# Optimization experiments

Measured on AMD Instinct MI355X. Metric: run time of the kernel, lower is better.

The kernel has to match this reference:

```python
import jax, jax.numpy as jnp
from jax import lax
import numpy as np

NPOINT = 2048
NSAMPLE = 16
LEAKY = 0.1


def _leaky(x):
    return jnp.where(x >= 0, x, LEAKY * x)


def _fps(pts, npoint):
    # pts: [B, N, 3] -> idx [B, npoint] (furthest point sampling, start at index 0)
    B, N, _ = pts.shape

    def step(carry, _):
        dist, far = carry  # dist [B,N], far [B]
        c = jnp.take_along_axis(pts, far[:, None, None], axis=1)  # [B,1,3]
        d = jnp.sum((pts - c) ** 2, -1)  # [B,N]
        dist = jnp.minimum(dist, d)
        nxt = jnp.argmax(dist, -1).astype(jnp.int32)
        return (dist, nxt), far

    init = (jnp.full((B, N), 1e10, pts.dtype), jnp.zeros((B,), jnp.int32))
    _, idx = lax.scan(step, init, None, length=npoint)
    return jnp.transpose(idx)  # [B, npoint]


def setup_inputs() -> dict:
    key = jax.random.key(0)
    ks = jax.random.split(key, 6)
    B, N, D, O = 8, 8192, 64, 128
    xyz = jax.random.normal(ks[0], (B, 3, N), jnp.float32)
    points = jax.random.normal(ks[1], (B, D, N), jnp.float32)
    W_kernel = jax.random.normal(ks[2], (O, D + 3), jnp.float32) * 0.05
    W_linear = jax.random.normal(ks[3], (O + NSAMPLE, O + NSAMPLE), jnp.float32) * 0.05
    W_point = jax.random.normal(ks[4], (NSAMPLE, NSAMPLE), jnp.float32) * 0.05
    W_channel = jax.random.normal(ks[5], (O, O), jnp.float32) * 0.05
    return {"xyz": xyz, "points": points, "W_kernel": W_kernel,
            "W_linear": W_linear, "W_point": W_point, "W_channel": W_channel}


def reference(xyz, points, W_kernel, W_linear, W_point, W_channel):
    K, S = NSAMPLE, NPOINT
    xyz_t = jnp.transpose(xyz, (0, 2, 1))      # [B,N,3]
    pts_t = jnp.transpose(points, (0, 2, 1))   # [B,N,D]

    fps_idx = _fps(xyz_t, S)                   # [B,S]
    new_xyz = jax.vmap(lambda p, i: p[i])(xyz_t, fps_idx)  # [B,S,3]

    # KNN: squared distances new_xyz -> xyz
    d = (jnp.sum(new_xyz ** 2, -1)[:, :, None]
         + jnp.sum(xyz_t ** 2, -1)[:, None, :]
         - 2.0 * jnp.einsum('bsc,bnc->bsn', new_xyz, xyz_t))  # [B,S,N]
    _, knn = lax.top_k(-d, K)                  # [B,S,K]

    gxyz = jax.vmap(lambda p, i: p[i])(xyz_t, knn)          # [B,S,K,3]
    gxyz_n = gxyz - new_xyz[:, :, None, :]
    gpts = jax.vmap(lambda p, i: p[i])(pts_t, knn)          # [B,S,K,D]
    new_points = jnp.concatenate([gxyz_n, gpts], -1)        # [B,S,K,3+D]

    # 1x1 conv2d kernel + LeakyReLU
    feat = _leaky(jnp.einsum('oc,bskc->bosk', W_kernel, new_points))  # [B,O,S,K]

    ch_avg = jnp.mean(feat, -1)                # [B,O,S]
    pt_avg = jnp.mean(feat, 1)                 # [B,S,K]
    agg = jnp.concatenate([ch_avg, jnp.transpose(pt_avg, (0, 2, 1))], 1)  # [B,O+K,S]
    agg = _leaky(jnp.einsum('oc,bcs->bos', W_linear, agg))

    wp = jax.nn.sigmoid(jnp.einsum('oc,bcs->bos', W_point, agg[:, -K:]))   # [B,K,S]
    wc = jax.nn.sigmoid(jnp.einsum('oc,bcs->bos', W_channel, agg[:, :-K]))  # [B,O,S]

    gated = feat * wc[:, :, :, None] * jnp.transpose(wp, (0, 2, 1))[:, None, :, :]
    out = jnp.mean(gated, -1)                  # [B,O,S]
    return jnp.transpose(new_xyz, (0, 2, 1)), out, fps_idx
```

## Files before the change

kernel.cpp:

```cpp
#include <hip/hip_runtime.h>
#include <stdint.h>

#define NB 8
#define NPT 8192
#define ND 64
#define NO 128
#define NS 2048
#define NK 16
#define NCONS 248
#define NITER 67

typedef float f32x2 __attribute__((ext_vector_type(2)));

constexpr int WS_PTS_T  = 0;
constexpr int WS_XYZW   = WS_PTS_T + NB*NPT*ND;
constexpr int WS_GFAR   = WS_XYZW + NB*NPT*4;
constexpr int WS_SYNC   = WS_GFAR + NB*NS;

constexpr int OUT_NEWXYZ = 0;
constexpr int OUT_FEAT   = NB*3*NS;
constexpr int OUT_FPS    = OUT_FEAT + NB*NO*NS;

__device__ __forceinline__ float sq3(float x, float y, float z) {
#pragma clang fp contract(off)
  return (x*x + y*y) + z*z;
}

__device__ __forceinline__ f32x2 fps_d2(f32x2 px, f32x2 py, f32x2 pz, f32x2 cx, f32x2 cy, f32x2 cz) {
#pragma clang fp contract(off)
  f32x2 dx = px - cx, dy = py - cy, dz = pz - cz;
  return (dx*dx + dy*dy) + dz*dz;
}

__device__ __forceinline__ float knn_d(float qn, float pn,
                                       float qx,float qy,float qz,
                                       float px,float py,float pz) {
#pragma clang fp contract(off)
  float dot = (qx*px + qy*py) + qz*pz;
  return (qn + pn) - 2.0f*dot;
}

__device__ __forceinline__ float wave_max_dpp(float x) {
  int v;
  v = __builtin_amdgcn_update_dpp(__float_as_int(x), __float_as_int(x), 0x111, 0xF, 0xF, false);
  x = fmaxf(x, __int_as_float(v));
  v = __builtin_amdgcn_update_dpp(__float_as_int(x), __float_as_int(x), 0x112, 0xF, 0xF, false);
  x = fmaxf(x, __int_as_float(v));
  v = __builtin_amdgcn_update_dpp(__float_as_int(x), __float_as_int(x), 0x114, 0xF, 0xF, false);
  x = fmaxf(x, __int_as_float(v));
  v = __builtin_amdgcn_update_dpp(__float_as_int(x), __float_as_int(x), 0x118, 0xF, 0xF, false);
  x = fmaxf(x, __int_as_float(v));
  v = __builtin_amdgcn_update_dpp(__float_as_int(x), __float_as_int(x), 0x142, 0xA, 0xF, false);
  x = fmaxf(x, __int_as_float(v));
  v = __builtin_amdgcn_update_dpp(__float_as_int(x), __float_as_int(x), 0x143, 0xC, 0xF, false);
  x = fmaxf(x, __int_as_float(v));
  return x;
}

__global__ void k_init(float* __restrict__ ws) {
  if (threadIdx.x < 9*32) ((int*)(ws + WS_SYNC))[threadIdx.x] = 0;
}

struct MegaShared {
  union {
    struct {
      float lx[NPT], ly[NPT], lz[NPT];
      unsigned long long wred[2][8];
    } f;
    struct { float tile[64][65]; } tr;
    struct {
      float W[128*69];
      union {
        float dist[NPT];
        struct { float np[16*69]; float ft[16*132]; float chred[256]; float ptred[16*17]; } p2;
      } u;
      unsigned long long kred[8];
      int selIdx[16];
      float agg[144];
      float a2[144];
      float gates[144];
    } c;
  } u;
};

__global__ __launch_bounds__(512) void k_mega(const float* __restrict__ xyz,
                                              const float* __restrict__ points,
                                              const float* __restrict__ Wkern,
                                              const float* __restrict__ Wlin,
                                              const float* __restrict__ Wpt,
                                              const float* __restrict__ Wch,
                                              float* __restrict__ ws,
                                              float* __restrict__ dout) {
  __shared__ MegaShared sh;
  const int bid = blockIdx.x, t = threadIdx.x;
  int* syncp = (int*)(ws + WS_SYNC);
  int* gfar  = (int*)(ws + WS_GFAR);

  if (bid < NB) {
    const float* xb = xyz + (size_t)bid*3*NPT;
    f32x2 px2[8], py2[8], pz2[8], dist2[8];
    const int base = t << 4;
#pragma unroll
    for (int jj = 0; jj < 4; jj++) {
      float4 vx = *reinterpret_cast<const float4*>(xb + base + jj*4);
      float4 vy = *reinterpret_cast<const float4*>(xb + NPT + base + jj*4);
      float4 vz = *reinterpret_cast<const float4*>(xb + 2*NPT + base + jj*4);
      px2[jj*2+0] = f32x2{vx.x, vx.y}; px2[jj*2+1] = f32x2{vx.z, vx.w};
      py2[jj*2+0] = f32x2{vy.x, vy.y}; py2[jj*2+1] = f32x2{vy.z, vy.w};
      pz2[jj*2+0] = f32x2{vz.x, vz.y}; pz2[jj*2+1] = f32x2{vz.z, vz.w};
      dist2[jj*2+0] = f32x2{1e10f, 1e10f}; dist2[jj*2+1] = f32x2{1e10f, 1e10f};
      sh.u.f.lx[base+jj*4+0]=vx.x; sh.u.f.lx[base+jj*4+1]=vx.y; sh.u.f.lx[base+jj*4+2]=vx.z; sh.u.f.lx[base+jj*4+3]=vx.w;
      sh.u.f.ly[base+jj*4+0]=vy.x; sh.u.f.ly[base+jj*4+1]=vy.y; sh.u.f.ly[base+jj*4+2]=vy.z; sh.u.f.ly[base+jj*4+3]=vy.w;
      sh.u.f.lz[base+jj*4+0]=vz.x; sh.u.f.lz[base+jj*4+1]=vz.y; sh.u.f.lz[base+jj*4+2]=vz.z; sh.u.f.lz[base+jj*4+3]=vz.w;
    }
    __syncthreads();

    int far = 0;
    int* gfb = gfar + (size_t)bid*NS;

    for (int s = 0; s < NS; s++) {
      float cx = sh.u.f.lx[far], cy = sh.u.f.ly[far], cz = sh.u.f.lz[far];
      if (t == 0) {
        gfb[s] = far;
        if ((s & 31) == 31)
          __hip_atomic_store(&syncp[bid*32], s+1, __ATOMIC_RELEASE, __HIP_MEMORY_SCOPE_AGENT);
      }
      const f32x2 c2x = {cx, cx}, c2y = {cy, cy}, c2z = {cz, cz};
      float bv = -1.0f; int bi = base;
#pragma unroll
      for (int j = 0; j < 8; j++) {
        f32x2 dd = fps_d2(px2[j], py2[j], pz2[j], c2x, c2y, c2z);
        float n0 = fminf(dist2[j].x, dd.x);
        float n1 = fminf(dist2[j].y, dd.y);
        dist2[j].x = n0; dist2[j].y = n1;
        if (n0 > bv) { bv = n0; bi = base + 2*j; }
        if (n1 > bv) { bv = n1; bi = base + 2*j + 1; }
      }
      float wm = wave_max_dpp(bv);
      float wmax = __int_as_float(__builtin_amdgcn_readlane(__float_as_int(wm), 63));
      unsigned long long eq = __ballot(bv == wmax);
      int winner = __ffsll((unsigned long long)eq) - 1;
      int wbi = __builtin_amdgcn_readlane(bi, winner);
      const int par = s & 1;
      if ((t & 63) == 0)
        sh.u.f.wred[par][t >> 6] = ((unsigned long long)__float_as_uint(wmax) << 32) | (unsigned)wbi;
      __syncthreads();
      unsigned long long best = sh.u.f.wred[par][0];
#pragma unroll
      for (int w = 1; w < 8; w++) {
        unsigned long long k2 = sh.u.f.wred[par][w];
        if ((unsigned)(k2 >> 32) > (unsigned)(best >> 32)) best = k2;
      }
      far = (int)(best & 0xFFFFFFFFull);
    }
    if (t == 0)
      __hip_atomic_store(&syncp[bid*32], NS, __ATOMIC_RELEASE, __HIP_MEMORY_SCOPE_AGENT);
    return;
  }

  const int cbid = bid - NB;

  for (int tile = cbid; tile < 1024; tile += NCONS) {
    const int b  = tile >> 7;
    const int n0 = (tile & 127) << 6;
    const float* pb = points + (size_t)b*ND*NPT;
    {
      int dR = t >> 3, cg = t & 7;
      const float* src = pb + (size_t)dR*NPT + n0 + cg*8;
      float4 v0 = *reinterpret_cast<const float4*>(src);
      float4 v1 = *reinterpret_cast<const float4*>(src + 4);
      sh.u.tr.tile[dR][cg*8+0]=v0.x; sh.u.tr.tile[dR][cg*8+1]=v0.y;
      sh.u.tr.tile[dR][cg*8+2]=v0.z; sh.u.tr.tile[dR][cg*8+3]=v0.w;
      sh.u.tr.tile[dR][cg*8+4]=v1.x; sh.u.tr.tile[dR][cg*8+5]=v1.y;
      sh.u.tr.tile[dR][cg*8+6]=v1.z; sh.u.tr.tile[dR][cg*8+7]=v1.w;
    }
    __syncthreads();
    {
      int nl = t >> 3, dg = t & 7;
      float4 w0, w1;
      w0.x = sh.u.tr.tile[dg*8+0][nl]; w0.y = sh.u.tr.tile[dg*8+1][nl];
      w0.z = sh.u.tr.tile[dg*8+2][nl]; w0.w = sh.u.tr.tile[dg*8+3][nl];
      w1.x = sh.u.tr.tile[dg*8+4][nl]; w1.y = sh.u.tr.tile[dg*8+5][nl];
      w1.z = sh.u.tr.tile[dg*8+6][nl]; w1.w = sh.u.tr.tile[dg*8+7][nl];
      float* dst = ws + WS_PTS_T + ((size_t)b*NPT + n0 + nl)*ND + dg*8;
      *reinterpret_cast<float4*>(dst)     = w0;
      *reinterpret_cast<float4*>(dst + 4) = w1;
    }
    __syncthreads();
  }
  for (int chunk = cbid; chunk < 128; chunk += NCONS) {
    int g = chunk*512 + t;
    int b = g >> 13, n = g & 8191;
    const float* xb = xyz + (size_t)b*3*NPT;
    float x = xb[n], y = xb[NPT+n], z = xb[2*NPT+n];
    float4 v; v.x=x; v.y=y; v.z=z; v.w=sq3(x,y,z);
    *reinterpret_cast<float4*>(ws + WS_XYZW + (size_t)g*4) = v;
  }
  __syncthreads();
  if (t == 0) {
    __hip_atomic_fetch_add(&syncp[8*32], 1, __ATOMIC_ACQ_REL, __HIP_MEMORY_SCOPE_AGENT);
    while (__hip_atomic_load(&syncp[8*32], __ATOMIC_RELAXED, __HIP_MEMORY_SCOPE_AGENT) < NCONS)
      __builtin_amdgcn_s_sleep(8);
    (void)__hip_atomic_load(&syncp[8*32], __ATOMIC_ACQUIRE, __HIP_MEMORY_SCOPE_AGENT);
  }
  __syncthreads();

  for (int g = t; g < 128*67; g += 512) {
    int o = g / 67, c = g - o*67;
    sh.u.c.W[o*69+c] = Wkern[g];
  }
  __syncthreads();

  for (int j = 0; j < NITER; j++) {
    const int i = cbid + j*NCONS;
    const bool active = (i < NB*NS);
    const int ii = active ? i : (NB*NS - 1);
    const int b = ii & 7, s = ii >> 3;

    if (t == 0) {
      while (__hip_atomic_load(&syncp[b*32], __ATOMIC_RELAXED, __HIP_MEMORY_SCOPE_AGENT) < s+1)
        __builtin_amdgcn_s_sleep(8);
      (void)__hip_atomic_load(&syncp[b*32], __ATOMIC_ACQUIRE, __HIP_MEMORY_SCOPE_AGENT);
    }
    __syncthreads();

    const float* xyzw = ws + WS_XYZW + (size_t)b*NPT*4;
    const int far = gfar[(size_t)b*NS + s];
    const float4 q = *reinterpret_cast<const float4*>(xyzw + (size_t)far*4);

    if (active) {
      if (t == 3) dout[OUT_FPS + (size_t)b*NS + s] = (float)far;
      else if (t < 3) dout[OUT_NEWXYZ + (size_t)b*3*NS + (size_t)t*NS + s] = (t==0) ? q.x : (t==1) ? q.y : q.z;
    }

#pragma unroll
    for (int i2 = 0; i2 < 16; i2++) {
      int n = t + (i2 << 9);
      float4 p = *reinterpret_cast<const float4*>(xyzw + (size_t)n*4);
      sh.u.c.u.dist[n] = knn_d(q.w, p.w, q.x, q.y, q.z, p.x, p.y, p.z);
    }
    __syncthreads();

    for (int r = 0; r < NK; r++) {
      float bv = __int_as_float(0x7F800000); int bi = NPT;
#pragma unroll
      for (int i2 = 0; i2 < 16; i2++) {
        int n = t + (i2 << 9);
        float v = sh.u.c.u.dist[n];
        if (v < bv) { bv = v; bi = n; }
      }
      unsigned uu = __float_as_uint(bv);
      uu ^= ((unsigned)((int)uu >> 31)) | 0x80000000u;
      unsigned long long key = ((unsigned long long)uu << 32) | (unsigned)bi;
#pragma unroll
      for (int m = 1; m < 64; m <<= 1) {
        unsigned long long o = __shfl_xor(key, m, 64);
        key = (o < key) ? o : key;
      }
      if ((t & 63) == 0) sh.u.c.kred[t >> 6] = key;
      __syncthreads();
      if (t == 0) {
        unsigned long long kmin = sh.u.c.kred[0];
#pragma unroll
        for (int w = 1; w < 8; w++) { unsigned long long o = sh.u.c.kred[w]; if (o < kmin) kmin = o; }
        int win = (int)(kmin & 0xFFFFFFFFull);
        sh.u.c.selIdx[r] = win;
        sh.u.c.u.dist[win] = __int_as_float(0x7F800000);
      }
      __syncthreads();
    }

    if (t < 256) {
      int k = t >> 4, cg = t & 15;
      int idx = sh.u.c.selIdx[k];
      float4 f = *reinterpret_cast<const float4*>(ws + WS_PTS_T + ((size_t)b*NPT + idx)*ND + cg*4);
      float* nprow = sh.u.c.u.p2.np + k*69;
      nprow[3+cg*4+0]=f.x; nprow[3+cg*4+1]=f.y; nprow[3+cg*4+2]=f.z; nprow[3+cg*4+3]=f.w;
      if (cg == 0) {
        float4 g4 = *reinterpret_cast<const float4*>(xyzw + (size_t)idx*4);
        nprow[0]=g4.x-q.x; nprow[1]=g4.y-q.y; nprow[2]=g4.z-q.z;
      }
    }
    __syncthreads();

    if (t < 256) {
      const int o = t & 127, khalf = t >> 7, k0 = khalf*8;
      float acc[8] = {0,0,0,0,0,0,0,0};
      const float* Wrow = sh.u.c.W + o*69;
      for (int c = 0; c < 67; c++) {
        float w = Wrow[c];
#pragma unroll
        for (int kk = 0; kk < 8; kk++)
          acc[kk] = fmaf(w, sh.u.c.u.p2.np[(k0+kk)*69 + c], acc[kk]);
      }
      float chp = 0.f;
#pragma unroll
      for (int kk = 0; kk < 8; kk++) {
        float a = acc[kk]; a = (a >= 0.f) ? a : 0.1f*a;
        sh.u.c.u.p2.ft[(k0+kk)*132 + o] = a; chp += a;
      }
      sh.u.c.u.p2.chred[khalf*128 + o] = chp;
    }
    __syncthreads();

    if (t < 128) sh.u.c.agg[t] = (sh.u.c.u.p2.chred[t] + sh.u.c.u.p2.chred[128+t]) * 0.0625f;
    if (t < 256) {
      int k = t & 15, og = t >> 4;
      float pp = 0.f;
#pragma unroll
      for (int jj = 0; jj < 8; jj++) pp += sh.u.c.u.p2.ft[k*132 + og*8 + jj];
      sh.u.c.u.p2.ptred[k*17 + og] = pp;
    }
    __syncthreads();
    if (t < 16) {
      float pv = 0.f;
#pragma unroll
      for (int og = 0; og < 16; og++) pv += sh.u.c.u.p2.ptred[t*17 + og];
      sh.u.c.agg[128 + t] = pv * 0.0078125f;
    }
    __syncthreads();

    if (t < 144) {
      float a = 0.f;
      const float* wr = Wlin + t*144;
      for (int c = 0; c < 144; c++) a = fmaf(wr[c], sh.u.c.agg[c], a);
      sh.u.c.a2[t] = (a >= 0.f) ? a : 0.1f*a;
    }
    __syncthreads();

    if (t < 128) {
      float a = 0.f;
      const float* wr = Wch + t*128;
      for (int c = 0; c < 128; c++) a = fmaf(wr[c], sh.u.c.a2[c], a);
      sh.u.c.gates[t] = 1.f / (1.f + expf(-a));
    } else if (t < 144) {
      int o = t - 128;
      float a = 0.f;
      const float* wr = Wpt + o*16;
      for (int c = 0; c < 16; c++) a = fmaf(wr[c], sh.u.c.a2[128+c], a);
      sh.u.c.gates[t] = 1.f / (1.f + expf(-a));
    }
    __syncthreads();

    if (t < 128 && active) {
      float sum = 0.f;
#pragma unroll
      for (int k = 0; k < 16; k++)
        sum = fmaf(sh.u.c.u.p2.ft[k*132 + t], sh.u.c.gates[128 + k], sum);
      dout[OUT_FEAT + ((size_t)b*NO + t)*NS + s] = sum * sh.u.c.gates[t] * 0.0625f;
    }
    __syncthreads();
  }
}

extern "C" void kernel_launch(void* const* d_in, const int* in_sizes, int n_in,
                              void* d_out, int out_size, void* d_ws, size_t ws_size,
                              hipStream_t stream) {
  (void)in_sizes; (void)n_in; (void)out_size; (void)ws_size;
  const float* xyz    = (const float*)d_in[0];
  const float* points = (const float*)d_in[1];
  const float* Wk     = (const float*)d_in[2];
  const float* Wl     = (const float*)d_in[3];
  const float* Wp     = (const float*)d_in[4];
  const float* Wc     = (const float*)d_in[5];
  float* ws  = (float*)d_ws;
  float* out = (float*)d_out;

  hipLaunchKernelGGL(k_init, dim3(1), dim3(512), 0, stream, ws);

  void* args[] = { (void*)&xyz, (void*)&points, (void*)&Wk, (void*)&Wl,
                   (void*)&Wp, (void*)&Wc, (void*)&ws, (void*)&out };
  hipLaunchCooperativeKernel(reinterpret_cast<void*>(k_mega),
                             dim3(NB + NCONS), dim3(512), args, 0, stream);
}
```

Baseline: 2.048 ms.

## Streamline FPS loop and signal consumers per sample via sentinel-initialized index array

The FPS producer now stores each selected index directly with a relaxed atomic into a gfar array pre-filled with -1. Consumers poll that slot instead of a batched counter, so they can start on each sample as soon as it exists rather than waiting for groups of 32. The FPS inner loop also changes: coordinates are kept as float4 records in LDS, a plain max reduction is followed by a separate argmax pass, and the cross-wave reduction uses DPP plus a ballot instead of a serial loop. Risks include memory-ordering subtleties from relaxed publishing and changed tie-breaking semantics.

```diff
diff --git a/kernel.cpp b/kernel.cpp
--- a/kernel.cpp
+++ b/kernel.cpp
@@ -57,14 +57,27 @@
   return x;
 }
 
+__device__ __forceinline__ float dpp8_max(float x) {
+  int v;
+  v = __builtin_amdgcn_update_dpp(__float_as_int(x), __float_as_int(x), 0x111, 0xF, 0xF, false);
+  x = fmaxf(x, __int_as_float(v));
+  v = __builtin_amdgcn_update_dpp(__float_as_int(x), __float_as_int(x), 0x112, 0xF, 0xF, false);
+  x = fmaxf(x, __int_as_float(v));
+  v = __builtin_amdgcn_update_dpp(__float_as_int(x), __float_as_int(x), 0x114, 0xF, 0xF, false);
+  x = fmaxf(x, __int_as_float(v));
+  return x;
+}
+
 __global__ void k_init(float* __restrict__ ws) {
-  if (threadIdx.x < 9*32) ((int*)(ws + WS_SYNC))[threadIdx.x] = 0;
+  int idx = blockIdx.x*512 + threadIdx.x;
+  if (idx < NB*NS) ((int*)(ws + WS_GFAR))[idx] = -1;
+  if (idx < 32)    ((int*)(ws + WS_SYNC))[idx] = 0;
 }
 
 struct MegaShared {
   union {
     struct {
-      float lx[NPT], ly[NPT], lz[NPT];
+      float lxyz[NPT][4];
       unsigned long long wred[2][8];
     } f;
     struct { float tile[64][65]; } tr;
@@ -79,6 +92,7 @@
       float agg[144];
       float a2[144];
       float gates[144];
+      int farSlot;
     } c;
   } u;
 };
@@ -109,9 +123,14 @@
       py2[jj*2+0] = f32x2{vy.x, vy.y}; py2[jj*2+1] = f32x2{vy.z, vy.w};
       pz2[jj*2+0] = f32x2{vz.x, vz.y}; pz2[jj*2+1] = f32x2{vz.z, vz.w};
       dist2[jj*2+0] = f32x2{1e10f, 1e10f}; dist2[jj*2+1] = f32x2{1e10f, 1e10f};
-      sh.u.f.lx[base+jj*4+0]=vx.x; sh.u.f.lx[base+jj*4+1]=vx.y; sh.u.f.lx[base+jj*4+2]=vx.z; sh.u.f.lx[base+jj*4+3]=vx.w;
-      sh.u.f.ly[base+jj*4+0]=vy.x; sh.u.f.ly[base+jj*4+1]=vy.y; sh.u.f.ly[base+jj*4+2]=vy.z; sh.u.f.ly[base+jj*4+3]=vy.w;
-      sh.u.f.lz[base+jj*4+0]=vz.x; sh.u.f.lz[base+jj*4+1]=vz.y; sh.u.f.lz[base+jj*4+2]=vz.z; sh.u.f.lz[base+jj*4+3]=vz.w;
+      float xs[4] = {vx.x, vx.y, vx.z, vx.w};
+      float ys[4] = {vy.x, vy.y, vy.z, vy.w};
+      float zs[4] = {vz.x, vz.y, vz.z, vz.w};
+#pragma unroll
+      for (int i = 0; i < 4; i++) {
+        float4 rec; rec.x = xs[i]; rec.y = ys[i]; rec.z = zs[i]; rec.w = 0.f;
+        *reinterpret_cast<float4*>(&sh.u.f.lxyz[base + jj*4 + i][0]) = rec;
+      }
     }
     __syncthreads();
 
@@ -119,22 +138,29 @@
     int* gfb = gfar + (size_t)bid*NS;
 
     for (int s = 0; s < NS; s++) {
-      float cx = sh.u.f.lx[far], cy = sh.u.f.ly[far], cz = sh.u.f.lz[far];
-      if (t == 0) {
-        gfb[s] = far;
-        if ((s & 31) == 31)
-          __hip_atomic_store(&syncp[bid*32], s+1, __ATOMIC_RELEASE, __HIP_MEMORY_SCOPE_AGENT);
-      }
-      const f32x2 c2x = {cx, cx}, c2y = {cy, cy}, c2z = {cz, cz};
-      float bv = -1.0f; int bi = base;
+      if (t == 0)
+        __hip_atomic_store(&gfb[s], far, __ATOMIC_RELAXED, __HIP_MEMORY_SCOPE_AGENT);
+
+      const float4 c4 = *reinterpret_cast<const float4*>(&sh.u.f.lxyz[far][0]);
+      const f32x2 c2x = {c4.x, c4.x}, c2y = {c4.y, c4.y}, c2z = {c4.z, c4.z};
+
+      f32x2 vmax2 = {-1.0f, -1.0f};
 #pragma unroll
       for (int j = 0; j < 8; j++) {
         f32x2 dd = fps_d2(px2[j], py2[j], pz2[j], c2x, c2y, c2z);
-        float n0 = fminf(dist2[j].x, dd.x);
-        float n1 = fminf(dist2[j].y, dd.y);
-        dist2[j].x = n0; dist2[j].y = n1;
-        if (n0 > bv) { bv = n0; bi = base + 2*j; }
-        if (n1 > bv) { bv = n1; bi = base + 2*j + 1; }
+        f32x2 nd;
+        nd.x = fminf(dist2[j].x, dd.x);
+        nd.y = fminf(dist2[j].y, dd.y);
+        dist2[j] = nd;
+        vmax2.x = fmaxf(vmax2.x, nd.x);
+        vmax2.y = fmaxf(vmax2.y, nd.y);
+      }
+      float bv = fmaxf(vmax2.x, vmax2.y);
+      int bi = base;
+#pragma unroll
+      for (int j = 7; j >= 0; --j) {
+        if (dist2[j].y == bv) bi = base + 2*j + 1;
+        if (dist2[j].x == bv) bi = base + 2*j;
       }
       float wm = wave_max_dpp(bv);
       float wmax = __int_as_float(__builtin_amdgcn_readlane(__float_as_int(wm), 63));
@@ -145,16 +171,16 @@
       if ((t & 63) == 0)
         sh.u.f.wred[par][t >> 6] = ((unsigned long long)__float_as_uint(wmax) << 32) | (unsigned)wbi;
       __syncthreads();
-      unsigned long long best = sh.u.f.wred[par][0];
-#pragma unroll
-      for (int w = 1; w < 8; w++) {
-        unsigned long long k2 = sh.u.f.wred[par][w];
-        if ((unsigned)(k2 >> 32) > (unsigned)(best >> 32)) best = k2;
-      }
-      far = (int)(best & 0xFFFFFFFFull);
-    }
-    if (t == 0)
-      __hip_atomic_store(&syncp[bid*32], NS, __ATOMIC_RELEASE, __HIP_MEMORY_SCOPE_AGENT);
+      {
+        unsigned long long kk = sh.u.f.wred[par][t & 7];
+        float sv = __int_as_float((int)(unsigned)(kk >> 32));
+        float sm = dpp8_max(sv);
+        float M = __int_as_float(__builtin_amdgcn_readlane(__float_as_int(sm), 7));
+        unsigned long long eqm = __ballot(sv == M) & 0xFFull;
+        int wwin = __ffsll(eqm) - 1;
+        far = __builtin_amdgcn_readlane((int)(kk & 0xFFFFFFFFull), wwin);
+      }
+    }
     return;
   }
 
@@ -198,10 +224,10 @@
   }
   __syncthreads();
   if (t == 0) {
-    __hip_atomic_fetch_add(&syncp[8*32], 1, __ATOMIC_ACQ_REL, __HIP_MEMORY_SCOPE_AGENT);
-    while (__hip_atomic_load(&syncp[8*32], __ATOMIC_RELAXED, __HIP_MEMORY_SCOPE_AGENT) < NCONS)
+    __hip_atomic_fetch_add(&syncp[0], 1, __ATOMIC_ACQ_REL, __HIP_MEMORY_SCOPE_AGENT);
+    while (__hip_atomic_load(&syncp[0], __ATOMIC_RELAXED, __HIP_MEMORY_SCOPE_AGENT) < NCONS)
       __builtin_amdgcn_s_sleep(8);
-    (void)__hip_atomic_load(&syncp[8*32], __ATOMIC_ACQUIRE, __HIP_MEMORY_SCOPE_AGENT);
+    (void)__hip_atomic_load(&syncp[0], __ATOMIC_ACQUIRE, __HIP_MEMORY_SCOPE_AGENT);
   }
   __syncthreads();
 
@@ -218,14 +244,15 @@
     const int b = ii & 7, s = ii >> 3;
 
     if (t == 0) {
-      while (__hip_atomic_load(&syncp[b*32], __ATOMIC_RELAXED, __HIP_MEMORY_SCOPE_AGENT) < s+1)
+      int f;
+      while ((f = __hip_atomic_load(&gfar[(size_t)b*NS + s], __ATOMIC_RELAXED, __HIP_MEMORY_SCOPE_AGENT)) == -1)
         __builtin_amdgcn_s_sleep(8);
-      (void)__hip_atomic_load(&syncp[b*32], __ATOMIC_ACQUIRE, __HIP_MEMORY_SCOPE_AGENT);
-    }
-    __syncthreads();
+      sh.u.c.farSlot = f;
+    }
+    __syncthreads();
+    const int far = sh.u.c.farSlot;
 
     const float* xyzw = ws + WS_XYZW + (size_t)b*NPT*4;
-    const int far = gfar[(size_t)b*NS + s];
     const float4 q = *reinterpret_cast<const float4*>(xyzw + (size_t)far*4);
 
     if (active) {
@@ -366,7 +393,7 @@
   float* ws  = (float*)d_ws;
   float* out = (float*)d_out;
 
-  hipLaunchKernelGGL(k_init, dim3(1), dim3(512), 0, stream, ws);
+  hipLaunchKernelGGL(k_init, dim3(32), dim3(512), 0, stream, ws);
 
   void* args[] = { (void*)&xyz, (void*)&points, (void*)&Wk, (void*)&Wl,
                    (void*)&Wp, (void*)&Wc, (void*)&ws, (void*)&out };
```

Measured after the change: 1.965 ms. 4.1% less time.
